# Optimization experiments

Measured on AMD Instinct MI355X. Metric: run time of the kernel, lower is better.

## Reference

```python
import jax, jax.numpy as jnp
import numpy as np

B, N, T, C, H, K = 2, 32, 512, 64, 4, 3
PAD = K - 1  # causal left-padding along time
HD = C // H


def setup_inputs() -> dict:
    key = jax.random.key(0)
    ks = jax.random.split(key, 9)
    s = 1.0 / np.sqrt(C)
    return {
        "values": jax.random.normal(ks[0], (B, N, T, C), jnp.float32),
        "keys": jax.random.normal(ks[1], (B, N, T, C), jnp.float32),
        "query": jax.random.normal(ks[2], (B, N, T, C), jnp.float32),
        "Wq": jax.random.normal(ks[3], (C, C, K, 1), jnp.float32) * s,  # Conv2d (out,in,k,1)
        "bq": jax.random.normal(ks[4], (C,), jnp.float32) * s,
        "Wk": jax.random.normal(ks[5], (C, C, K, 1), jnp.float32) * s,
        "bk": jax.random.normal(ks[6], (C,), jnp.float32) * s,
        "Wv": jax.random.normal(ks[7], (C, C), jnp.float32) * s,  # 1x1 conv, no bias
        "Wf": jax.random.normal(ks[8], (C, C), jnp.float32) * s,  # Linear (out,in)
        "bf": jnp.zeros((C,), jnp.float32),
    }


def _causal_conv(x, w, b):
    # x: (B,N,T,C) -> NCHW (B,C,T,N); kernel (k,1) over T with left pad = K-1 (causal)
    xp = jnp.transpose(x, (0, 3, 2, 1))
    y = jax.lax.conv_general_dilated(
        xp, w, window_strides=(1, 1), padding=[(PAD, 0), (0, 0)],
        dimension_numbers=("NCHW", "OIHW", "NCHW"))
    y = y + b[None, :, None, None]
    return jnp.transpose(y, (0, 3, 2, 1))  # back to (B,N,T,C)


def reference(values, keys, query, Wq, bq, Wk, bk, Wv, Wf, bf):
    q = _causal_conv(query, Wq, bq).reshape(B, N, T, H, HD)
    k = _causal_conv(keys, Wk, bk).reshape(B, N, T, H, HD)
    v = jnp.einsum("bntc,oc->bnto", values, Wv).reshape(B, N, T, H, HD)  # 1x1 conv
    energy = jnp.einsum("bnqhd,bnkhd->bnqkh", q, k)  # (B,N,T,T,H)
    attn = jax.nn.softmax(energy / np.sqrt(C).astype(np.float32), axis=3)
    out = jnp.einsum("bnqkh,bnkhd->bnqhd", attn, v).reshape(B, N, T, C)
    return out @ Wf.T + bf
```

## Files before the change

### kernel.cpp

```cpp
#include <hip/hip_runtime.h>

#define DEVI __device__ __forceinline__

typedef __attribute__((ext_vector_type(8)))  short s16x8;
typedef __attribute__((ext_vector_type(4)))  short s16x4;
typedef __attribute__((ext_vector_type(4)))  float f32x4;
typedef __attribute__((ext_vector_type(16))) float f32x16;
typedef __attribute__((ext_vector_type(2)))  unsigned u32x2;
typedef __attribute__((ext_vector_type(4)))  unsigned u32x4;

DEVI short f2bf(float f) {
  unsigned u = __builtin_bit_cast(unsigned, f);
  u = u + 0x7fffu + ((u >> 16) & 1u);
  return (short)(u >> 16);
}
DEVI unsigned cvtpk(float lo, float hi) {
  unsigned r;
  asm("v_cvt_pk_bf16_f32 %0, %1, %2" : "=v"(r) : "v"(lo), "v"(hi));
  return r;
}
DEVI void gll16(const short* g, short* l) {
  __builtin_amdgcn_global_load_lds(
      (const __attribute__((address_space(1))) unsigned*)g,
      (__attribute__((address_space(3))) unsigned*)l, 16, 0, 0);
}

constexpr int TT = 512;
constexpr int CC = 64;
constexpr float SCLQ = 0.18033688011112042f;

__global__ __launch_bounds__(256) void k_qkv(const float* __restrict__ values,
                                             const float* __restrict__ keys,
                                             const float* __restrict__ query,
                                             const float* __restrict__ Wq,
                                             const float* __restrict__ bq,
                                             const float* __restrict__ Wk,
                                             const float* __restrict__ bk,
                                             const float* __restrict__ Wv,
                                             short* __restrict__ qg,
                                             short* __restrict__ kgF,
                                             short* __restrict__ vgT) {
  __shared__ __align__(16) short smem[16896];
  short* lx = smem;
  const int idx = blockIdx.x;
  const int xcd = idx & 7, rest = idx >> 3;
  const int tsr = rest >> 6;
  const int rr = rest & 63;
  const int bn = xcd * 8 + (rr >> 3), t8 = rr & 7;
  const int t0 = t8 * 64;
  const size_t xbase = (size_t)bn * TT * CC;
  const int tid = threadIdx.x;
  const int lane = tid & 63, w = tid >> 6;
  const int r = lane & 31, hl = lane >> 5;

  const float* in = (tsr == 0) ? query : (tsr == 1) ? keys : values;
  const int nrows = (tsr < 2) ? 66 : 64;
  const int halo = (tsr < 2) ? 2 : 0;
  short* lw = (tsr < 2) ? (smem + 4224) : (smem + 8320);
  short* lxT = smem + 4224;

  if (tsr < 2) {
    const float* wsrc = tsr ? Wk : Wq;
    for (int s = tid; s < 4096; s += 256) {
      lw[s]        = f2bf(wsrc[s * 3 + 0]);
      lw[4096 + s] = f2bf(wsrc[s * 3 + 1]);
      lw[8192 + s] = f2bf(wsrc[s * 3 + 2]);
    }
  } else {
    for (int s = tid; s < 4096; s += 256) lw[s] = f2bf(Wv[s]);
  }

  for (int s = tid; s < nrows * 8; s += 256) {
    int row = s >> 3, c8 = s & 7;
    int t = t0 - halo + row;
    u32x4 rv;
    if (t >= 0) {
      const float4 a = *(const float4*)(in + xbase + (size_t)t * 64 + c8 * 8);
      const float4 b = *(const float4*)(in + xbase + (size_t)t * 64 + c8 * 8 + 4);
      rv[0] = cvtpk(a.x, a.y); rv[1] = cvtpk(a.z, a.w);
      rv[2] = cvtpk(b.x, b.y); rv[3] = cvtpk(b.z, b.w);
    } else {
      rv = (u32x4)(0u);
    }
    int byte = row * 128 + ((c8 * 16) ^ ((row & 7) << 4));
    *(u32x4*)((char*)lx + byte) = rv;
  }
  __syncthreads();

  {
    int mt = w >> 1, nt = w & 1;
    f32x16 acc;
#pragma unroll
    for (int i = 0; i < 16; ++i) acc[i] = 0.f;

    if (tsr < 2) {
#pragma unroll
      for (int kk = 0; kk < 3; ++kk) {
#pragma unroll
        for (int c4 = 0; c4 < 4; ++c4) {
          int lrow = mt * 32 + r + kk;
          int abyte = lrow * 128 + (((c4 * 16 + hl * 8) * 2) ^ ((lrow & 7) << 4));
          s16x8 af = *(const s16x8*)((const char*)lx + abyte);
          s16x8 bfr = *(const s16x8*)(lw + kk * 4096 + (nt * 32 + r) * 64 + c4 * 16 + hl * 8);
          acc = __builtin_amdgcn_mfma_f32_32x32x16_bf16(af, bfr, acc, 0, 0, 0);
        }
      }
    } else {
#pragma unroll
      for (int c4 = 0; c4 < 4; ++c4) {
        int lrow = mt * 32 + r;
        int abyte = lrow * 128 + (((c4 * 16 + hl * 8) * 2) ^ ((lrow & 7) << 4));
        s16x8 af = *(const s16x8*)((const char*)lx + abyte);
        s16x8 bfr = *(const s16x8*)(lw + (nt * 32 + r) * 64 + c4 * 16 + hl * 8);
        acc = __builtin_amdgcn_mfma_f32_32x32x16_bf16(af, bfr, acc, 0, 0, 0);
      }
    }
    int co = nt * 32 + r;
    if (tsr == 2) {
#pragma unroll
      for (int g2 = 0; g2 < 4; ++g2) {
        int tl = mt * 32 + g2 * 8 + hl * 4;
        u32x2 pk;
        pk[0] = cvtpk(acc[g2 * 4 + 0], acc[g2 * 4 + 1]);
        pk[1] = cvtpk(acc[g2 * 4 + 2], acc[g2 * 4 + 3]);
        *(u32x2*)(lxT + co * 64 + (tl ^ ((co & 15) << 2))) = pk;
      }
    } else if (tsr == 0) {
      float bias = bq[co];
#pragma unroll
      for (int reg = 0; reg < 16; ++reg) {
        int trow = mt * 32 + (reg & 3) + 8 * (reg >> 2) + 4 * hl;
        qg[((size_t)bn * TT + (t0 + trow)) * 64 + co] = f2bf((acc[reg] + bias) * SCLQ);
      }
    } else {
      float bias = bk[co];
      int h = co >> 4, ch = co & 15;
      short* kb = kgF + ((size_t)bn * 4 + h) * 8192 + (ch >> 3) * 256 + (ch & 7);
#pragma unroll
      for (int reg = 0; reg < 16; ++reg) {
        int t = t0 + mt * 32 + (reg & 3) + 8 * (reg >> 2) + 4 * hl;
        kb[(t >> 5) * 512 + (t & 31) * 8] = f2bf(acc[reg] + bias);
      }
    }
  }
  if (tsr == 2) {
    __syncthreads();
#pragma unroll
    for (int i = 0; i < 4; ++i) {
      int chunk = tid + 256 * i;
      int co = chunk >> 4, tc = chunk & 15;
      s16x4 v4 = *(const s16x4*)(lxT + co * 64 + ((tc * 4) ^ ((co & 15) << 2)));
      *(s16x4*)(vgT + ((size_t)bn * 64 + co) * TT + t0 + tc * 4) = v4;
    }
  }
}

__global__ __launch_bounds__(256, 4) void k_attn(const short* __restrict__ qg,
                                                 const short* __restrict__ kgF,
                                                 const short* __restrict__ vgT,
                                                 short* __restrict__ ag) {
  __shared__ __align__(16) short Vl[16 * 512];
  __shared__ float Sums[4][32];
  const int tid = threadIdx.x;
  const int b = (blockIdx.x & 7) * 128 + (blockIdx.x >> 3);
  const int bn = b >> 4, h = (b >> 2) & 3, qq = b & 3;
  const int lane = tid & 63, w = tid >> 6;
  const int r = lane & 31, hl = lane >> 5;

  const short* vslice = vgT + ((size_t)bn * 64 + h * 16) * TT;
#pragma unroll
  for (int j = 0; j < 4; ++j) {
    int d = j * 256 + tid;
    int ch = d >> 6, tc = (d & 63) ^ (ch & 7);
    gll16(vslice + (size_t)ch * TT + tc * 8, Vl + d * 8);
  }

  const int mt = qq * 4 + w;
  s16x8 qf = *(const s16x8*)(qg + ((size_t)bn * TT + mt * 32 + r) * CC + h * 16 + hl * 8);
  const short* kgh = kgF + ((size_t)bn * 4 + h) * 8192 + lane * 8;
  const int vch = r & 15;
  const char* vrow = (const char*)Vl + vch * 1024;

  __syncthreads();

  f32x16 z;
#pragma unroll
  for (int i = 0; i < 16; ++i) z[i] = 0.f;
  float sm0 = 0.f, sm1 = 0.f, sm2 = 0.f, sm3 = 0.f;
  f32x16 o;
#pragma unroll
  for (int i = 0; i < 16; ++i) o[i] = 0.f;

#pragma unroll
  for (int nt = 0; nt < 16; ++nt) {
    s16x8 kf = *(const s16x8*)(kgh + nt * 512);
    f32x16 s = __builtin_amdgcn_mfma_f32_32x32x16_bf16(kf, qf, z, 0, 0, 0);
    float p[16];
#pragma unroll
    for (int i = 0; i < 16; ++i)
      p[i] = fmaxf(__builtin_amdgcn_exp2f(s[i]), 0.f);
#pragma unroll
    for (int i = 0; i < 4; ++i) {
      sm0 += p[4 * i + 0]; sm1 += p[4 * i + 1];
      sm2 += p[4 * i + 2]; sm3 += p[4 * i + 3];
    }
    unsigned pk[8];
#pragma unroll
    for (int m = 0; m < 8; ++m) pk[m] = cvtpk(p[2 * m], p[2 * m + 1]);
#pragma unroll
    for (int s2 = 0; s2 < 2; ++s2) {
      unsigned a0 = pk[4 * s2 + 0], b0 = pk[4 * s2 + 2];
      unsigned a1 = pk[4 * s2 + 1], b1 = pk[4 * s2 + 3];
      asm("v_permlane32_swap_b32 %0, %1" : "+v"(a0), "+v"(b0));
      asm("v_permlane32_swap_b32 %0, %1" : "+v"(a1), "+v"(b1));
      u32x4 fw; fw[0] = a0; fw[1] = a1; fw[2] = b0; fw[3] = b1;
      s16x8 fr = __builtin_bit_cast(s16x8, fw);
      s16x8 vf = *(const s16x8*)(vrow + (((nt * 32 + s2 * 16 + hl * 8) * 2) ^ ((vch & 7) << 4)));
      o = __builtin_amdgcn_mfma_f32_32x32x16_bf16(fr, vf, o, 0, 0, 0);
    }
  }
  float sum = (sm0 + sm1) + (sm2 + sm3);
  sum += __shfl_xor(sum, 32);
  Sums[w][r] = sum;
  if (r < 16) {
#pragma unroll
    for (int reg = 0; reg < 16; ++reg) {
      int qlocal = (reg & 3) + 8 * (reg >> 2) + 4 * hl;
      float inv = __builtin_amdgcn_rcpf(Sums[w][qlocal]);
      int q = mt * 32 + qlocal;
      ag[((size_t)bn * TT + q) * CC + h * 16 + r] = f2bf(o[reg] * inv);
    }
  }
}

__global__ __launch_bounds__(256) void k_out(const short* __restrict__ ag,
                                             const float* __restrict__ Wf,
                                             const float* __restrict__ bfv,
                                             float* __restrict__ out) {
  __shared__ __align__(16) short la[64 * 64];
  __shared__ __align__(16) short lw[64 * 64];
  const int tid = threadIdx.x;
  const int xcd = blockIdx.x & 7, rest = blockIdx.x >> 3;
  const int bn = xcd * 8 + (rest >> 3), t8 = rest & 7;
  const int t0 = t8 * 64;
#pragma unroll
  for (int j = 0; j < 2; ++j) {
    int d = j * 256 + tid;
    int row = d >> 3, c8 = (d & 7) ^ (row & 7);
    gll16(ag + ((size_t)bn * TT + t0 + row) * 64 + c8 * 8, la + d * 8);
  }
  for (int s = tid; s < 4096; s += 256) lw[s] = f2bf(Wf[s]);
  __syncthreads();
  const int lane = tid & 63, w = tid >> 6;
  const int r = lane & 31, hl = lane >> 5;
  {
    int mt = w >> 1, nt = w & 1;
    f32x16 acc;
#pragma unroll
    for (int i = 0; i < 16; ++i) acc[i] = 0.f;
#pragma unroll
    for (int c4 = 0; c4 < 4; ++c4) {
      int lrow = mt * 32 + r;
      int abyte = lrow * 128 + (((c4 * 16 + hl * 8) * 2) ^ ((lrow & 7) << 4));
      s16x8 af = *(const s16x8*)((const char*)la + abyte);
      s16x8 bfr = *(const s16x8*)(lw + (nt * 32 + r) * 64 + c4 * 16 + hl * 8);
      acc = __builtin_amdgcn_mfma_f32_32x32x16_bf16(af, bfr, acc, 0, 0, 0);
    }
    int co = nt * 32 + r;
    float bias = bfv[co];
#pragma unroll
    for (int reg = 0; reg < 16; ++reg) {
      int trow = mt * 32 + (reg & 3) + 8 * (reg >> 2) + 4 * hl;
      out[((size_t)bn * TT + t0 + trow) * 64 + co] = acc[reg] + bias;
    }
  }
}

extern "C" void kernel_launch(void* const* d_in, const int* in_sizes, int n_in,
                              void* d_out, int out_size, void* d_ws, size_t ws_size,
                              hipStream_t stream) {
  const float* values = (const float*)d_in[0];
  const float* keys = (const float*)d_in[1];
  const float* query = (const float*)d_in[2];
  const float* Wq = (const float*)d_in[3];
  const float* bq = (const float*)d_in[4];
  const float* Wk = (const float*)d_in[5];
  const float* bk = (const float*)d_in[6];
  const float* Wv = (const float*)d_in[7];
  const float* Wf = (const float*)d_in[8];
  const float* bfv = (const float*)d_in[9];
  float* out = (float*)d_out;

  char* ws = (char*)d_ws;
  short* qg = (short*)ws;
  short* kgF = (short*)(ws + (1 << 22));
  short* vgT = (short*)(ws + 2 * (1 << 22));
  short* ag = (short*)(ws + 3 * (size_t)(1 << 22));

  hipLaunchKernelGGL(k_qkv, dim3(1536), dim3(256), 0, stream,
                     values, keys, query, Wq, bq, Wk, bk, Wv, qg, kgF, vgT);
  hipLaunchKernelGGL(k_attn, dim3(1024), dim3(256), 0, stream, qg, kgF, vgT, ag);
  hipLaunchKernelGGL(k_out, dim3(512), dim3(256), 0, stream, ag, Wf, bfv, out);
}
```

Before: 38.47 us.

## Fuse attention and output projection into one 1024-thread kernel

```diff
diff --git a/kernel.cpp b/kernel.cpp
--- a/kernel.cpp
+++ b/kernel.cpp
@@ -155,30 +155,36 @@
   }
 }
 
-__global__ __launch_bounds__(256, 4) void k_attn(const short* __restrict__ qg,
-                                                 const short* __restrict__ kgF,
-                                                 const short* __restrict__ vgT,
-                                                 short* __restrict__ ag) {
-  __shared__ __align__(16) short Vl[16 * 512];
-  __shared__ float Sums[4][32];
+__global__ __launch_bounds__(1024) void k_attn_out(const short* __restrict__ qg,
+                                                   const short* __restrict__ kgF,
+                                                   const short* __restrict__ vgT,
+                                                   const float* __restrict__ Wf,
+                                                   const float* __restrict__ bfv,
+                                                   float* __restrict__ out) {
+  __shared__ __align__(16) short Vl[64 * 512];
+  __shared__ __align__(16) short la[128 * 64];
+  __shared__ __align__(16) short lw[64 * 64];
+  __shared__ float Sums[16][32];
   const int tid = threadIdx.x;
-  const int b = (blockIdx.x & 7) * 128 + (blockIdx.x >> 3);
-  const int bn = b >> 4, h = (b >> 2) & 3, qq = b & 3;
-  const int lane = tid & 63, w = tid >> 6;
+  const int xcd = blockIdx.x & 7, rest = blockIdx.x >> 3;
+  const int bn = xcd * 8 + (rest >> 2), qq = rest & 3;
+  const int lane = tid & 63, w16 = tid >> 6;
+  const int h = w16 & 3, mtl = w16 >> 2;
   const int r = lane & 31, hl = lane >> 5;
 
-  const short* vslice = vgT + ((size_t)bn * 64 + h * 16) * TT;
+  const short* vslice = vgT + (size_t)bn * 64 * TT;
 #pragma unroll
   for (int j = 0; j < 4; ++j) {
-    int d = j * 256 + tid;
+    int d = j * 1024 + tid;
     int ch = d >> 6, tc = (d & 63) ^ (ch & 7);
     gll16(vslice + (size_t)ch * TT + tc * 8, Vl + d * 8);
   }
-
-  const int mt = qq * 4 + w;
+  for (int s = tid; s < 4096; s += 1024) lw[s] = f2bf(Wf[s]);
+
+  const int mt = qq * 4 + mtl;
   s16x8 qf = *(const s16x8*)(qg + ((size_t)bn * TT + mt * 32 + r) * CC + h * 16 + hl * 8);
   const short* kgh = kgF + ((size_t)bn * 4 + h) * 8192 + lane * 8;
-  const int vch = r & 15;
+  const int vch = h * 16 + (r & 15);
   const char* vrow = (const char*)Vl + vch * 1024;
 
   __syncthreads();
@@ -221,46 +227,28 @@
   }
   float sum = (sm0 + sm1) + (sm2 + sm3);
   sum += __shfl_xor(sum, 32);
-  Sums[w][r] = sum;
+  Sums[w16][r] = sum;
   if (r < 16) {
 #pragma unroll
     for (int reg = 0; reg < 16; ++reg) {
       int qlocal = (reg & 3) + 8 * (reg >> 2) + 4 * hl;
-      float inv = __builtin_amdgcn_rcpf(Sums[w][qlocal]);
-      int q = mt * 32 + qlocal;
-      ag[((size_t)bn * TT + q) * CC + h * 16 + r] = f2bf(o[reg] * inv);
-    }
-  }
-}
-
-__global__ __launch_bounds__(256) void k_out(const short* __restrict__ ag,
-                                             const float* __restrict__ Wf,
-                                             const float* __restrict__ bfv,
-                                             float* __restrict__ out) {
-  __shared__ __align__(16) short la[64 * 64];
-  __shared__ __align__(16) short lw[64 * 64];
-  const int tid = threadIdx.x;
-  const int xcd = blockIdx.x & 7, rest = blockIdx.x >> 3;
-  const int bn = xcd * 8 + (rest >> 3), t8 = rest & 7;
-  const int t0 = t8 * 64;
-#pragma unroll
-  for (int j = 0; j < 2; ++j) {
-    int d = j * 256 + tid;
-    int row = d >> 3, c8 = (d & 7) ^ (row & 7);
-    gll16(ag + ((size_t)bn * TT + t0 + row) * 64 + c8 * 8, la + d * 8);
-  }
-  for (int s = tid; s < 4096; s += 256) lw[s] = f2bf(Wf[s]);
+      float inv = __builtin_amdgcn_rcpf(Sums[w16][qlocal]);
+      int row = mtl * 32 + qlocal;
+      int col = h * 16 + r;
+      *(short*)((char*)la + row * 128 + (((col >> 3) * 16) ^ ((row & 7) << 4)) + (col & 7) * 2) =
+          f2bf(o[reg] * inv);
+    }
+  }
   __syncthreads();
-  const int lane = tid & 63, w = tid >> 6;
-  const int r = lane & 31, hl = lane >> 5;
-  {
-    int mt = w >> 1, nt = w & 1;
+
+  if (w16 < 8) {
+    int mt2 = w16 >> 1, nt = w16 & 1;
     f32x16 acc;
 #pragma unroll
     for (int i = 0; i < 16; ++i) acc[i] = 0.f;
 #pragma unroll
     for (int c4 = 0; c4 < 4; ++c4) {
-      int lrow = mt * 32 + r;
+      int lrow = mt2 * 32 + r;
       int abyte = lrow * 128 + (((c4 * 16 + hl * 8) * 2) ^ ((lrow & 7) << 4));
       s16x8 af = *(const s16x8*)((const char*)la + abyte);
       s16x8 bfr = *(const s16x8*)(lw + (nt * 32 + r) * 64 + c4 * 16 + hl * 8);
@@ -270,8 +258,8 @@
     float bias = bfv[co];
 #pragma unroll
     for (int reg = 0; reg < 16; ++reg) {
-      int trow = mt * 32 + (reg & 3) + 8 * (reg >> 2) + 4 * hl;
-      out[((size_t)bn * TT + t0 + trow) * 64 + co] = acc[reg] + bias;
+      int trow = mt2 * 32 + (reg & 3) + 8 * (reg >> 2) + 4 * hl;
+      out[((size_t)bn * TT + qq * 128 + trow) * CC + co] = acc[reg] + bias;
     }
   }
 }
@@ -295,10 +283,9 @@
   short* qg = (short*)ws;
   short* kgF = (short*)(ws + (1 << 22));
   short* vgT = (short*)(ws + 2 * (1 << 22));
-  short* ag = (short*)(ws + 3 * (size_t)(1 << 22));
 
   hipLaunchKernelGGL(k_qkv, dim3(1536), dim3(256), 0, stream,
                      values, keys, query, Wq, bq, Wk, bk, Wv, qg, kgF, vgT);
-  hipLaunchKernelGGL(k_attn, dim3(1024), dim3(256), 0, stream, qg, kgF, vgT, ag);
-  hipLaunchKernelGGL(k_out, dim3(512), dim3(256), 0, stream, ag, Wf, bfv, out);
-}
+  hipLaunchKernelGGL(k_attn_out, dim3(256), dim3(1024), 0, stream,
+                     qg, kgF, vgT, Wf, bfv, out);
+}
```

Result: faster. 34.96 us (median of 2 runs) (-9.1%).
